# Optimization experiments

Measured on AMD Instinct MI355X. Metric: run time of the kernel, lower is better.

The kernel has to match this reference:

```python
import jax, jax.numpy as jnp
import numpy as np

N = 1281167        # memory bank size (ImageNet train set)
NEGS = 4096        # negatives per sample
PROJ_DIM = 128
TEMPERATURE = 0.07
BATCH = 256


def setup_inputs() -> dict:
    key = jax.random.key(0)
    k1, k2, k3, k4 = jax.random.split(key, 4)
    proj = jax.random.normal(k1, (BATCH, PROJ_DIM), dtype=jnp.float32)
    proj = proj / jnp.linalg.norm(proj, axis=-1, keepdims=True)
    bank = jax.random.normal(k2, (N, PROJ_DIM), dtype=jnp.float32)
    bank = bank / jnp.linalg.norm(bank, axis=-1, keepdims=True)
    pos_index = jax.random.randint(k3, (BATCH,), 0, N)
    idx = jax.random.randint(k4, (BATCH, NEGS + 1), 0, N)
    idx = idx.at[:, 0].set(pos_index)  # first column is the positive sample
    return {"proj": proj, "bank": bank, "idx": idx}


def reference(proj, bank, idx):
    # gather (negs+1) bank rows per batch element: [B, negs+1, D]
    samples = bank[idx]
    # batched dot product: [B, negs+1]
    sim = jnp.einsum('bkd,bd->bk', samples, proj)
    out = jnp.exp(sim / TEMPERATURE)
    # z is estimated once from the first batch and treated as a constant
    z = jax.lax.stop_gradient(out.mean()) * N
    output = out / z
    m = NEGS / N  # noise prior ratio Pn(i)*negs
    p_d = jnp.log(output[:, 0] / (output[:, 0] + m))          # [B]
    p_n = jnp.log(m / (output[:, 1:] + m))                    # [B, negs]
    loss = -(p_d.sum() + p_n.sum()) / BATCH
    pos_samples = samples[:, 0]                               # [B, D]
    return loss, pos_samples
```

## Files before the change

kernel.cpp:

```cpp
#include <hip/hip_runtime.h>
#include <math.h>

#define N_BANK   1281167
#define NEGS     4096
#define K_TOT    (NEGS + 1)
#define PROJ_DIM 128
#define BATCH    256
#define CHUNKS   8
#define KCH      ((K_TOT + CHUNKS - 1) / CHUNKS)

__global__ __launch_bounds__(256) void npid_main(
    const float* __restrict__ proj, const float* __restrict__ bank,
    const int* __restrict__ idx, float* __restrict__ out,
    float* __restrict__ expv, double* __restrict__ accum)
{
    const int b     = blockIdx.x / CHUNKS;
    const int chunk = blockIdx.x % CHUNKS;
    const int tid   = threadIdx.x;
    const int group = tid >> 4;
    const int lane  = tid & 15;

    __shared__ int    sidx[KCH];
    __shared__ double sred[256];

    const int k0     = chunk * KCH;
    const int kcount = (k0 + KCH <= K_TOT) ? KCH : (K_TOT - k0);

    for (int t = tid; t < kcount; t += 256)
        sidx[t] = idx[b * K_TOT + k0 + t];
    __syncthreads();

    const float* pr = proj + b * PROJ_DIM;
    float4 p0 = *(const float4*)(pr + 4 * lane);
    float4 p1 = *(const float4*)(pr + 64 + 4 * lane);

    double dsum = 0.0;
    int j = group;
    for (; j + 16 < kcount; j += 32) {
        const int r0 = sidx[j];
        const int r1 = sidx[j + 16];
        const float* br0 = bank + (long long)r0 * PROJ_DIM;
        const float* br1 = bank + (long long)r1 * PROJ_DIM;
        float4 a0 = *(const float4*)(br0 + 4 * lane);
        float4 a1 = *(const float4*)(br0 + 64 + 4 * lane);
        float4 c0 = *(const float4*)(br1 + 4 * lane);
        float4 c1 = *(const float4*)(br1 + 64 + 4 * lane);

        float s0 = p0.x*a0.x + p0.y*a0.y + p0.z*a0.z + p0.w*a0.w
                 + p1.x*a1.x + p1.y*a1.y + p1.z*a1.z + p1.w*a1.w;
        float s1 = p0.x*c0.x + p0.y*c0.y + p0.z*c0.z + p0.w*c0.w
                 + p1.x*c1.x + p1.y*c1.y + p1.z*c1.z + p1.w*c1.w;

        s0 += __shfl_xor(s0, 1);  s1 += __shfl_xor(s1, 1);
        s0 += __shfl_xor(s0, 2);  s1 += __shfl_xor(s1, 2);
        s0 += __shfl_xor(s0, 4);  s1 += __shfl_xor(s1, 4);
        s0 += __shfl_xor(s0, 8);  s1 += __shfl_xor(s1, 8);

        if (lane == 0) {
            float e0 = expf(s0 * (1.0f / 0.07f));
            float e1 = expf(s1 * (1.0f / 0.07f));
            expv[b * K_TOT + k0 + j]      = e0;
            expv[b * K_TOT + k0 + j + 16] = e1;
            dsum += (double)e0 + (double)e1;
        }
    }
    if (j < kcount) {
        const int r0 = sidx[j];
        const float* br0 = bank + (long long)r0 * PROJ_DIM;
        float4 a0 = *(const float4*)(br0 + 4 * lane);
        float4 a1 = *(const float4*)(br0 + 64 + 4 * lane);
        float s0 = p0.x*a0.x + p0.y*a0.y + p0.z*a0.z + p0.w*a0.w
                 + p1.x*a1.x + p1.y*a1.y + p1.z*a1.z + p1.w*a1.w;
        s0 += __shfl_xor(s0, 1);
        s0 += __shfl_xor(s0, 2);
        s0 += __shfl_xor(s0, 4);
        s0 += __shfl_xor(s0, 8);
        if (lane == 0) {
            float e0 = expf(s0 * (1.0f / 0.07f));
            expv[b * K_TOT + k0 + j] = e0;
            dsum += (double)e0;
        }
    }

    if (chunk == 0 && group == 0) {
        const int row = sidx[0];
        const float* br = bank + (long long)row * PROJ_DIM;
        *(float4*)(out + 1 + b * PROJ_DIM + 4 * lane)      = *(const float4*)(br + 4 * lane);
        *(float4*)(out + 1 + b * PROJ_DIM + 64 + 4 * lane) = *(const float4*)(br + 64 + 4 * lane);
    }

    sred[tid] = dsum;
    __syncthreads();
    for (int off = 128; off > 0; off >>= 1) {
        if (tid < off) sred[tid] += sred[tid + off];
        __syncthreads();
    }
    if (tid == 0) atomicAdd(accum, sred[0]);
}

__global__ __launch_bounds__(256) void npid_loss(
    const float* __restrict__ expv, const double* __restrict__ accum,
    double* __restrict__ lossacc)
{
    const double z  = (accum[0] / (double)(BATCH * K_TOT)) * (double)N_BANK;
    const double mz = ((double)NEGS / (double)N_BANK) * z;
    const float inv_mz = (float)(1.0 / mz);

    const int nvec = (BATCH * K_TOT) / 4;
    const int i = blockIdx.x * blockDim.x + threadIdx.x;

    double local = 0.0;
    if (i < nvec) {
        float4 o = ((const float4*)expv)[i];
        float t = log1pf(o.x * inv_mz) + log1pf(o.y * inv_mz)
                + log1pf(o.z * inv_mz) + log1pf(o.w * inv_mz);
        local = -(double)t;
    }

    __shared__ double sred[256];
    const int tid = threadIdx.x;
    sred[tid] = local;
    __syncthreads();
    for (int off = 128; off > 0; off >>= 1) {
        if (tid < off) sred[tid] += sred[tid + off];
        __syncthreads();
    }
    if (tid == 0) atomicAdd(lossacc, sred[0]);
}

__global__ void npid_init(double* __restrict__ accum)
{
    if (threadIdx.x < 2) accum[threadIdx.x] = 0.0;
}

__global__ __launch_bounds__(256) void npid_final(
    const float* __restrict__ expv, const double* __restrict__ accum,
    const double* __restrict__ lossacc, float* __restrict__ out)
{
    const double z  = (accum[0] / (double)(BATCH * K_TOT)) * (double)N_BANK;
    const double mz = ((double)NEGS / (double)N_BANK) * z;

    const int b = threadIdx.x;
    const double o = (double)expv[b * K_TOT];
    double corr = log1p(o / mz) - log1p(mz / o);

    __shared__ double sred[256];
    sred[b] = corr;
    __syncthreads();
    for (int off = 128; off > 0; off >>= 1) {
        if (b < off) sred[b] += sred[b + off];
        __syncthreads();
    }
    if (b == 0)
        out[0] = (float)(-(lossacc[0] + sred[0]) / (double)BATCH);
}

extern "C" void kernel_launch(void* const* d_in, const int* in_sizes, int n_in,
                              void* d_out, int out_size, void* d_ws, size_t ws_size,
                              hipStream_t stream)
{
    const float* proj = (const float*)d_in[0];
    const float* bank = (const float*)d_in[1];
    const int*   idx  = (const int*)d_in[2];
    float* out = (float*)d_out;

    double* accum = (double*)d_ws;
    float*  expv  = (float*)((char*)d_ws + 16);

    npid_init <<<1, 64, 0, stream>>>(accum);
    npid_main <<<BATCH * CHUNKS, 256, 0, stream>>>(proj, bank, idx, out, expv, accum);
    const int nvec = (BATCH * K_TOT) / 4;
    npid_loss <<<(nvec + 255) / 256, 256, 0, stream>>>(expv, accum, accum + 1);
    npid_final<<<1, 256, 0, stream>>>(expv, accum, accum + 1, out);
}
```

Before: 107.9 us.

## Replace atomic accumulators with per-block partials, drop init kernel, double chunking

Global double atomics are replaced by per-block partial sums written to workspace, which the loss and final kernels reduce themselves. This removes the init kernel launch and the atomic contention. The main kernel now splits each batch row into 16 chunks instead of 8 for more blocks, and its tail loop becomes a loop so it handles any remainder. Block reductions now use wavefront shuffles instead of a shared-memory tree. In exchange, every loss block redundantly re-reads and sums the 4096 main partials.

Result: faster. 98.20 us (-9.0%).

```diff
diff --git a/kernel.cpp b/kernel.cpp
--- a/kernel.cpp
+++ b/kernel.cpp
@@ -6,22 +6,39 @@
 #define K_TOT    (NEGS + 1)
 #define PROJ_DIM 128
 #define BATCH    256
-#define CHUNKS   8
+#define CHUNKS   16
 #define KCH      ((K_TOT + CHUNKS - 1) / CHUNKS)
+#define GRID_MAIN (BATCH * CHUNKS)
+#define NVEC     ((BATCH * K_TOT) / 4)
+#define GRID_LOSS ((NVEC + 255) / 256)
+
+#define WS_MAINPART(ws) ((double*)(ws))
+#define WS_LOSSPART(ws) ((double*)((char*)(ws) + 32768))
+#define WS_EXPV(ws)     ((float*)((char*)(ws) + 65536))
+
+__device__ __forceinline__ double block_reduce_bcast(double v, double* swred, int tid)
+{
+    for (int off = 32; off > 0; off >>= 1) v += __shfl_down(v, off);
+    if ((tid & 63) == 0) swred[tid >> 6] = v;
+    __syncthreads();
+    double r = swred[0] + swred[1] + swred[2] + swred[3];
+    __syncthreads();
+    return r;
+}
 
 __global__ __launch_bounds__(256) void npid_main(
     const float* __restrict__ proj, const float* __restrict__ bank,
     const int* __restrict__ idx, float* __restrict__ out,
-    float* __restrict__ expv, double* __restrict__ accum)
+    float* __restrict__ expv, double* __restrict__ mainpart)
 {
-    const int b     = blockIdx.x / CHUNKS;
-    const int chunk = blockIdx.x % CHUNKS;
+    const int b     = blockIdx.x >> 4;
+    const int chunk = blockIdx.x & 15;
     const int tid   = threadIdx.x;
     const int group = tid >> 4;
     const int lane  = tid & 15;
 
     __shared__ int    sidx[KCH];
-    __shared__ double sred[256];
+    __shared__ double swred[4];
 
     const int k0     = chunk * KCH;
     const int kcount = (k0 + KCH <= K_TOT) ? KCH : (K_TOT - k0);
@@ -64,7 +81,7 @@
             dsum += (double)e0 + (double)e1;
         }
     }
-    if (j < kcount) {
+    for (; j < kcount; j += 16) {
         const int r0 = sidx[j];
         const float* br0 = bank + (long long)r0 * PROJ_DIM;
         float4 a0 = *(const float4*)(br0 + 4 * lane);
@@ -89,70 +106,60 @@
         *(float4*)(out + 1 + b * PROJ_DIM + 64 + 4 * lane) = *(const float4*)(br + 64 + 4 * lane);
     }
 
-    sred[tid] = dsum;
-    __syncthreads();
-    for (int off = 128; off > 0; off >>= 1) {
-        if (tid < off) sred[tid] += sred[tid + off];
-        __syncthreads();
-    }
-    if (tid == 0) atomicAdd(accum, sred[0]);
+    double bsum = block_reduce_bcast(dsum, swred, tid);
+    if (tid == 0) mainpart[blockIdx.x] = bsum;
 }
 
 __global__ __launch_bounds__(256) void npid_loss(
-    const float* __restrict__ expv, const double* __restrict__ accum,
-    double* __restrict__ lossacc)
+    const float* __restrict__ expv, const double* __restrict__ mainpart,
+    double* __restrict__ losspart)
 {
-    const double z  = (accum[0] / (double)(BATCH * K_TOT)) * (double)N_BANK;
+    const int tid = threadIdx.x;
+    __shared__ double swred[4];
+
+    double zs = 0.0;
+    for (int t = tid; t < GRID_MAIN; t += 256) zs += mainpart[t];
+    const double esum = block_reduce_bcast(zs, swred, tid);
+
+    const double z  = (esum / (double)(BATCH * K_TOT)) * (double)N_BANK;
     const double mz = ((double)NEGS / (double)N_BANK) * z;
     const float inv_mz = (float)(1.0 / mz);
 
-    const int nvec = (BATCH * K_TOT) / 4;
-    const int i = blockIdx.x * blockDim.x + threadIdx.x;
-
+    const int i = blockIdx.x * 256 + tid;
     double local = 0.0;
-    if (i < nvec) {
+    if (i < NVEC) {
         float4 o = ((const float4*)expv)[i];
         float t = log1pf(o.x * inv_mz) + log1pf(o.y * inv_mz)
                 + log1pf(o.z * inv_mz) + log1pf(o.w * inv_mz);
         local = -(double)t;
     }
 
-    __shared__ double sred[256];
-    const int tid = threadIdx.x;
-    sred[tid] = local;
-    __syncthreads();
-    for (int off = 128; off > 0; off >>= 1) {
-        if (tid < off) sred[tid] += sred[tid + off];
-        __syncthreads();
-    }
-    if (tid == 0) atomicAdd(lossacc, sred[0]);
-}
-
-__global__ void npid_init(double* __restrict__ accum)
-{
-    if (threadIdx.x < 2) accum[threadIdx.x] = 0.0;
+    double bsum = block_reduce_bcast(local, swred, tid);
+    if (tid == 0) losspart[blockIdx.x] = bsum;
 }
 
 __global__ __launch_bounds__(256) void npid_final(
-    const float* __restrict__ expv, const double* __restrict__ accum,
-    const double* __restrict__ lossacc, float* __restrict__ out)
+    const float* __restrict__ expv, const double* __restrict__ mainpart,
+    const double* __restrict__ losspart, float* __restrict__ out)
 {
-    const double z  = (accum[0] / (double)(BATCH * K_TOT)) * (double)N_BANK;
+    const int tid = threadIdx.x;
+    __shared__ double swred[4];
+
+    double zs = 0.0;
+    for (int t = tid; t < GRID_MAIN; t += 256) zs += mainpart[t];
+    const double esum = block_reduce_bcast(zs, swred, tid);
+
+    const double z  = (esum / (double)(BATCH * K_TOT)) * (double)N_BANK;
     const double mz = ((double)NEGS / (double)N_BANK) * z;
 
-    const int b = threadIdx.x;
-    const double o = (double)expv[b * K_TOT];
-    double corr = log1p(o / mz) - log1p(mz / o);
+    double lsum = 0.0;
+    for (int t = tid; t < GRID_LOSS; t += 256) lsum += losspart[t];
 
-    __shared__ double sred[256];
-    sred[b] = corr;
-    __syncthreads();
-    for (int off = 128; off > 0; off >>= 1) {
-        if (b < off) sred[b] += sred[b + off];
-        __syncthreads();
-    }
-    if (b == 0)
-        out[0] = (float)(-(lossacc[0] + sred[0]) / (double)BATCH);
+    const double o = (double)expv[tid * K_TOT];
+    lsum += log1p(o / mz) - log1p(mz / o);
+
+    double total = block_reduce_bcast(lsum, swred, tid);
+    if (tid == 0) out[0] = (float)(-total / (double)BATCH);
 }
 
 extern "C" void kernel_launch(void* const* d_in, const int* in_sizes, int n_in,
@@ -164,12 +171,11 @@
     const int*   idx  = (const int*)d_in[2];
     float* out = (float*)d_out;
 
-    double* accum = (double*)d_ws;
-    float*  expv  = (float*)((char*)d_ws + 16);
+    double* mainpart = WS_MAINPART(d_ws);
+    double* losspart = WS_LOSSPART(d_ws);
+    float*  expv     = WS_EXPV(d_ws);
 
-    npid_init <<<1, 64, 0, stream>>>(accum);
-    npid_main <<<BATCH * CHUNKS, 256, 0, stream>>>(proj, bank, idx, out, expv, accum);
-    const int nvec = (BATCH * K_TOT) / 4;
-    npid_loss <<<(nvec + 255) / 256, 256, 0, stream>>>(expv, accum, accum + 1);
-    npid_final<<<1, 256, 0, stream>>>(expv, accum, accum + 1, out);
+    npid_main <<<GRID_MAIN, 256, 0, stream>>>(proj, bank, idx, out, expv, mainpart);
+    npid_loss <<<GRID_LOSS, 256, 0, stream>>>(expv, mainpart, losspart);
+    npid_final<<<1, 256, 0, stream>>>(expv, mainpart, losspart, out);
 }
```
